# Kernel tuning notes

Measured on AMD Instinct MI355X. Metric: run time of the kernel, lower is better.

The kernel has to match this reference:

```python
import jax, jax.numpy as jnp
import numpy as np

B, S, D_IN, D_OUT, H = 4, 2048, 1024, 1024, 16
HD = D_OUT // H


def setup_inputs() -> dict:
    key = jax.random.key(0)
    ks = jax.random.split(key, 6)
    s = 1.0 / np.sqrt(D_IN)
    x = jax.random.normal(ks[0], (B, S, D_IN), dtype=jnp.float32)
    Wq = jax.random.uniform(ks[1], (D_OUT, D_IN), jnp.float32, -s, s)  # torch Linear weight [out,in]
    Wk = jax.random.uniform(ks[2], (D_OUT, D_IN), jnp.float32, -s, s)
    Wv = jax.random.uniform(ks[3], (D_OUT, D_IN), jnp.float32, -s, s)
    so = 1.0 / np.sqrt(D_OUT)
    Wo = jax.random.uniform(ks[4], (D_OUT, D_OUT), jnp.float32, -so, so)
    bo = jax.random.uniform(ks[5], (D_OUT,), jnp.float32, -so, so)
    return {"x": x, "Wq": Wq, "Wk": Wk, "Wv": Wv, "Wo": Wo, "bo": bo}


def reference(x, Wq, Wk, Wv, Wo, bo):
    b, n, _ = x.shape
    # projections (torch Linear: x @ W^T), split heads -> [b, h, n, hd]
    def heads(y):
        return y.reshape(b, n, H, HD).transpose(0, 2, 1, 3)
    q = heads(x @ Wq.T)
    k = heads(x @ Wk.T)
    v = heads(x @ Wv.T)
    scores = jnp.einsum('bhqd,bhkd->bhqk', q, k)
    causal = jnp.triu(jnp.ones((n, n), dtype=bool), k=1)
    scores = jnp.where(causal, -jnp.inf, scores)
    attn = jax.nn.softmax(scores / np.sqrt(HD), axis=-1)  # dropout p=0.0 -> identity
    ctx = jnp.einsum('bhqk,bhkd->bhqd', attn, v)
    ctx = ctx.transpose(0, 2, 1, 3).reshape(b, n, D_OUT)
    return ctx @ Wo.T + bo
```

## Files before the change

kernel.cpp:

```cpp
#include <hip/hip_runtime.h>
#include <hip/hip_bf16.h>
#include <stdint.h>

#define B_N 4
#define SEQ 2048
#define DMODEL 1024
#define NHEAD 16
#define HDIM 64
#define BHEADS (B_N * NHEAD)
#define MROWS (B_N * SEQ)

typedef short bf16x8_t __attribute__((ext_vector_type(8)));
typedef float f32x4_t __attribute__((ext_vector_type(4)));

static __device__ __forceinline__ unsigned short f2bf(float f) {
  __hip_bfloat16 h = __float2bfloat16(f);
  return __builtin_bit_cast(unsigned short, h);
}

#define GLDS16(gp, lp)                                                        \
  __builtin_amdgcn_global_load_lds(                                           \
      (const __attribute__((address_space(1))) unsigned int*)(gp),            \
      (__attribute__((address_space(3))) unsigned int*)(lp), 16, 0, 0)

__global__ void cast_f32_bf16_v4(const float* __restrict__ in,
                                 unsigned short* __restrict__ out, int n4,
                                 float scale) {
  int i = blockIdx.x * blockDim.x + threadIdx.x;
  if (i >= n4) return;
  float4 v = reinterpret_cast<const float4*>(in)[i];
  ushort4 o;
  o.x = f2bf(v.x * scale); o.y = f2bf(v.y * scale);
  o.z = f2bf(v.z * scale); o.w = f2bf(v.w * scale);
  reinterpret_cast<ushort4*>(out)[i] = o;
}

__global__ void cast_weights(const float* __restrict__ Wq,
                             const float* __restrict__ Wk,
                             const float* __restrict__ Wv,
                             const float* __restrict__ Wo,
                             unsigned short* __restrict__ out) {
  int i = blockIdx.x * blockDim.x + threadIdx.x;
  int mat = i >> 18;
  int off = i & 262143;
  const float* src = (mat == 0) ? Wq : (mat == 1) ? Wk : (mat == 2) ? Wv : Wo;
  float scale = (mat == 0) ? 0.125f : 1.0f;
  float4 v = reinterpret_cast<const float4*>(src)[off];
  ushort4 o;
  o.x = f2bf(v.x * scale); o.y = f2bf(v.y * scale);
  o.z = f2bf(v.z * scale); o.w = f2bf(v.w * scale);
  reinterpret_cast<ushort4*>(out)[i] = o;
}


#define SLOT_B 24576
#define NSLOT 5

#define GEMM_PIPE_LOOP(NHv)                                                   \
  int cur = 0, nxt = 3;                                                       \
  for (int h = 0; h < (NHv); ++h) {                                           \
    const char* cb = (const char*)smem + cur * SLOT_B;                        \
    bf16x8_t af[4], bfr[4];                                                   \
    _Pragma("unroll")                                                         \
    for (int rt = 0; rt < 4; rt++)                                            \
      af[rt] = *(const bf16x8_t*)(cb + offA[rt]);                             \
    _Pragma("unroll")                                                         \
    for (int ct = 0; ct < 4; ct++)                                            \
      bfr[ct] = *(const bf16x8_t*)(cb + offB[ct]);                            \
    if (h + 3 < (NHv)) {                                                      \
      char* sb = (char*)smem + nxt * SLOT_B;                                  \
      GLDS16(aB + (size_t)(h + 3) * 32, sb + t * 16);                         \
      GLDS16(b0B + (size_t)(h + 3) * 32, sb + 8192 + t * 16);                 \
      GLDS16(b1B + (size_t)(h + 3) * 32, sb + 16384 + t * 16);                \
    }                                                                         \
    __builtin_amdgcn_s_barrier();                                             \
    asm volatile("s_waitcnt lgkmcnt(0)" ::: "memory");                        \
    __builtin_amdgcn_s_setprio(1);                                            \
    _Pragma("unroll")                                                         \
    for (int rt = 0; rt < 4; rt++)                                            \
      _Pragma("unroll")                                                       \
      for (int ct = 0; ct < 4; ct++)                                          \
        acc[rt][ct] = __builtin_amdgcn_mfma_f32_16x16x32_bf16(                \
            af[rt], bfr[ct], acc[rt][ct], 0, 0, 0);                           \
    __builtin_amdgcn_s_setprio(0);                                            \
    if (h + 1 < (NHv)) {                                                      \
      if (h + 3 < (NHv))                                                      \
        asm volatile("s_waitcnt vmcnt(6)" ::: "memory");                      \
      else if (h + 2 < (NHv))                                                 \
        asm volatile("s_waitcnt vmcnt(3)" ::: "memory");                      \
      else                                                                    \
        asm volatile("s_waitcnt vmcnt(0)" ::: "memory");                      \
      __builtin_amdgcn_s_barrier();                                           \
    }                                                                         \
    if (++cur == NSLOT) cur = 0;                                              \
    if (++nxt == NSLOT) nxt = 0;                                              \
  }

__global__ __launch_bounds__(512, 2)
void gemm_qkv(const unsigned short* __restrict__ A,
              const unsigned short* __restrict__ W,
              unsigned short* __restrict__ Out) {
  __shared__ __align__(16) unsigned short smem[61440];

  const int t = threadIdx.x;
  const int lane = t & 63;
  const int w = t >> 6;
  const int quad = lane >> 4;
  const int l16 = lane & 15;
  const int rowBase = blockIdx.x * 128;
  const int colBase = blockIdx.y * 256;
  const int wr = (w >> 2) * 64;
  const int wc = (w & 3) * 64;
  const int K = DMODEL;
  const int NH = K / 32;

  const int srow = t >> 2;
  const int ssw = ((t & 3) ^ ((t >> 3) & 3)) * 8;
  const unsigned short* aB  = A + (size_t)(rowBase + srow) * K + ssw;
  const unsigned short* b0B = W + (size_t)(colBase + srow) * K + ssw;
  const unsigned short* b1B = W + (size_t)(colBase + 128 + srow) * K + ssw;

  const int swz = (quad ^ ((l16 >> 1) & 3)) * 16;
  int offA[4], offB[4];
#pragma unroll
  for (int rt = 0; rt < 4; rt++) offA[rt] = (wr + rt * 16 + l16) * 64 + swz;
#pragma unroll
  for (int ct = 0; ct < 4; ct++)
    offB[ct] = 8192 + (wc + ct * 16 + l16) * 64 + swz;

  f32x4_t zero4 = {0.f, 0.f, 0.f, 0.f};
  f32x4_t acc[4][4];
#pragma unroll
  for (int i = 0; i < 4; i++)
#pragma unroll
    for (int j = 0; j < 4; j++) acc[i][j] = zero4;

#pragma unroll
  for (int h = 0; h < 3; ++h) {
    char* sb = (char*)smem + h * SLOT_B;
    GLDS16(aB + h * 32, sb + t * 16);
    GLDS16(b0B + h * 32, sb + 8192 + t * 16);
    GLDS16(b1B + h * 32, sb + 16384 + t * 16);
  }
  asm volatile("s_waitcnt vmcnt(6)" ::: "memory");
  __builtin_amdgcn_s_barrier();

  GEMM_PIPE_LOOP(NH)

  __syncthreads();

  const int mat = colBase >> 10;
  const int nl = colBase & 1023;
  const int hh = (nl + wc) >> 6;
  const int bb = rowBase >> 11;

  if (mat == 2) {
    unsigned short* T = smem + w * 4608;
#pragma unroll
    for (int ct = 0; ct < 4; ct++)
#pragma unroll
      for (int rt = 0; rt < 4; rt++) {
        ushort4 pk;
        pk.x = f2bf(acc[rt][ct][0]);
        pk.y = f2bf(acc[rt][ct][1]);
        pk.z = f2bf(acc[rt][ct][2]);
        pk.w = f2bf(acc[rt][ct][3]);
        *(ushort4*)&T[(ct * 16 + l16) * 72 + rt * 16 + quad * 4] = pk;
      }
    const int srw = (rowBase & (SEQ - 1)) + wr;
    unsigned short* Cq = Out + 2 * (size_t)MROWS * DMODEL;
#pragma unroll
    for (int it = 0; it < 8; it++) {
      int nn = it * 8 + (lane >> 3);
      int sg = lane & 7;
      uint4 d = *(const uint4*)&T[nn * 72 + sg * 8];
      *(uint4*)(Cq + ((size_t)(bb * NHEAD + hh) * HDIM + nn) * SEQ + srw +
                sg * 8) = d;
    }
  } else {
    unsigned short* T = smem + w * 4608;
#pragma unroll
    for (int rt = 0; rt < 4; rt++)
#pragma unroll
      for (int ct = 0; ct < 4; ct++)
#pragma unroll
        for (int r = 0; r < 4; r++)
          T[(rt * 16 + quad * 4 + r) * 72 + ct * 16 + l16] =
              f2bf(acc[rt][ct][r]);
    unsigned short* Cq = Out + (size_t)mat * MROWS * DMODEL;
#pragma unroll
    for (int it = 0; it < 8; it++) {
      int idx = it * 64 + lane;
      int row = idx >> 3, sg = idx & 7, sgx = sg ^ (row & 7);
      uint4 d = *(const uint4*)&T[row * 72 + sgx * 8];
      int m = rowBase + wr + row;
      int s = m & (SEQ - 1), b = m >> 11;
      *(uint4*)(Cq + (((size_t)(b * NHEAD + hh)) * SEQ + s) * HDIM + sgx * 8) = d;
    }
  }
}

__global__ __launch_bounds__(512, 2)
void gemm_out(const unsigned short* __restrict__ A,
              const unsigned short* __restrict__ Bw,
              float* __restrict__ Cf, const float* __restrict__ bias) {
  __shared__ __align__(16) unsigned short smem[61440];

  const int t = threadIdx.x;
  const int lane = t & 63;
  const int w = t >> 6;
  const int quad = lane >> 4;
  const int l16 = lane & 15;
  const int rowBase = blockIdx.x * 128;
  const int colBase = blockIdx.y * 256;
  const int wr = (w >> 2) * 64;
  const int wc = (w & 3) * 64;
  const int K = DMODEL, N = DMODEL;
  const int NH = K / 32;

  const int srow = t >> 2;
  const int ssw = ((t & 3) ^ ((t >> 3) & 3)) * 8;
  const unsigned short* aB  = A + (size_t)(rowBase + srow) * K + ssw;
  const unsigned short* b0B = Bw + (size_t)(colBase + srow) * K + ssw;
  const unsigned short* b1B = Bw + (size_t)(colBase + 128 + srow) * K + ssw;

  const int swz = (quad ^ ((l16 >> 1) & 3)) * 16;
  int offA[4], offB[4];
#pragma unroll
  for (int rt = 0; rt < 4; rt++) offA[rt] = (wr + rt * 16 + l16) * 64 + swz;
#pragma unroll
  for (int ct = 0; ct < 4; ct++)
    offB[ct] = 8192 + (wc + ct * 16 + l16) * 64 + swz;

  f32x4_t zero4 = {0.f, 0.f, 0.f, 0.f};
  f32x4_t acc[4][4];
#pragma unroll
  for (int i = 0; i < 4; i++)
#pragma unroll
    for (int j = 0; j < 4; j++) acc[i][j] = zero4;

#pragma unroll
  for (int h = 0; h < 3; ++h) {
    char* sb = (char*)smem + h * SLOT_B;
    GLDS16(aB + h * 32, sb + t * 16);
    GLDS16(b0B + h * 32, sb + 8192 + t * 16);
    GLDS16(b1B + h * 32, sb + 16384 + t * 16);
  }
  asm volatile("s_waitcnt vmcnt(6)" ::: "memory");
  __builtin_amdgcn_s_barrier();

  GEMM_PIPE_LOOP(NH)

#pragma unroll
  for (int rt = 0; rt < 4; rt++)
#pragma unroll
    for (int ct = 0; ct < 4; ct++) {
      int n = colBase + wc + ct * 16 + l16;
      float bv = bias[n];
#pragma unroll
      for (int r = 0; r < 4; r++) {
        int m = rowBase + wr + rt * 16 + quad * 4 + r;
        Cf[(size_t)m * N + n] = acc[rt][ct][r] + bv;
      }
    }
}

__global__ __launch_bounds__(256, 3)
void attn_kernel(const unsigned short* __restrict__ Qg_,
                 const unsigned short* __restrict__ Kg_,
                 const unsigned short* __restrict__ Vtg_,
                 unsigned short* __restrict__ ctx) {
  __shared__ __align__(16) unsigned short Ks[2][4096];
  __shared__ __align__(16) unsigned short Vs[2][4096];
  __shared__ __align__(16) unsigned short Ps[4][2048];

  const int t = threadIdx.x;
  const int lane = t & 63, w = t >> 6;
  const int quad = lane >> 4, l16 = lane & 15;
  const int sw = l16 & 7;
  unsigned short* PsW = &Ps[w][0];

  const int rank = blockIdx.x;
  const int qt = 15 - (rank >> 6);
  const int bh = rank & 63;
  const int nt = 2 * qt + 2;
  const size_t base = (size_t)bh * SEQ * HDIM;

  const int r0 = t >> 3;
  const int s0 = ((t & 7) ^ (r0 & 7)) * 8;
  const int r1 = r0 + 32;

  const unsigned short* Kg = Kg_ + base;
  const unsigned short* Vg = Vtg_ + base;

  GLDS16(Kg + r0 * HDIM + s0, (char*)&Ks[0][0] + t * 16);
  GLDS16(Kg + r1 * HDIM + s0, (char*)&Ks[0][0] + t * 16 + 4096);
  GLDS16(Vg + (size_t)r0 * SEQ + s0, (char*)&Vs[0][0] + t * 16);
  GLDS16(Vg + (size_t)r1 * SEQ + s0, (char*)&Vs[0][0] + t * 16 + 4096);

  const int q0w = qt * 128 + w * 32;

  bf16x8_t qf[2][2];
#pragma unroll
  for (int q2 = 0; q2 < 2; q2++)
#pragma unroll
    for (int kh = 0; kh < 2; kh++)
      qf[q2][kh] = *(const bf16x8_t*)(Qg_ + base +
          (size_t)(q0w + q2 * 16 + l16) * HDIM + kh * 32 + quad * 8);

  float l_[2] = {0.f, 0.f};
  f32x4_t zero4 = {0.f, 0.f, 0.f, 0.f};
  f32x4_t o[2][4];
#pragma unroll
  for (int q2 = 0; q2 < 2; q2++)
#pragma unroll
    for (int dt = 0; dt < 4; dt++) o[q2][dt] = zero4;

  int buf = 0;
  for (int jt = 0; jt < nt; ++jt) {
    __syncthreads();
    if (jt + 1 < nt) {
      const unsigned short* Kg2 = Kg + (size_t)(jt + 1) * 64 * HDIM;
      const unsigned short* Vg2 = Vg + (jt + 1) * 64;
      char* kd = (char*)&Ks[buf ^ 1][0] + t * 16;
      char* vd = (char*)&Vs[buf ^ 1][0] + t * 16;
      GLDS16(Kg2 + r0 * HDIM + s0, kd);
      GLDS16(Kg2 + r1 * HDIM + s0, kd + 4096);
      GLDS16(Vg2 + (size_t)r0 * SEQ + s0, vd);
      GLDS16(Vg2 + (size_t)r1 * SEQ + s0, vd + 4096);
    }

    if (jt * 64 <= q0w + 31) {
      const unsigned short* Kb = &Ks[buf][0];
      const unsigned short* Vb = &Vs[buf][0];
      f32x4_t sc[2][4];
#pragma unroll
      for (int q2 = 0; q2 < 2; q2++)
#pragma unroll
        for (int kt = 0; kt < 4; kt++) sc[q2][kt] = zero4;

#pragma unroll
      for (int kt = 0; kt < 4; kt++)
#pragma unroll
        for (int kh = 0; kh < 2; kh++) {
          bf16x8_t kf = *(const bf16x8_t*)((const char*)Kb +
              ((kt * 16 + l16) * 64 + (((kh * 4 + quad) ^ sw) * 8)) * 2);
          sc[0][kt] = __builtin_amdgcn_mfma_f32_16x16x32_bf16(
              kf, qf[0][kh], sc[0][kt], 0, 0, 0);
          sc[1][kt] = __builtin_amdgcn_mfma_f32_16x16x32_bf16(
              kf, qf[1][kh], sc[1][kt], 0, 0, 0);
        }

      if (jt * 64 + 63 > q0w) {
#pragma unroll
        for (int q2 = 0; q2 < 2; q2++) {
          int q = q0w + q2 * 16 + l16;
#pragma unroll
          for (int kt = 0; kt < 4; kt++)
#pragma unroll
            for (int r = 0; r < 4; r++) {
              int key = jt * 64 + kt * 16 + quad * 4 + r;
              if (key > q) sc[q2][kt][r] = -3.0e38f;
            }
        }
      }

#pragma unroll
      for (int q2 = 0; q2 < 2; q2++) {
        float sum = 0.f;
#pragma unroll
        for (int kt = 0; kt < 4; kt++) {
          float p0 = __expf(sc[q2][kt][0]);
          float p1 = __expf(sc[q2][kt][1]);
          float p2 = __expf(sc[q2][kt][2]);
          float p3 = __expf(sc[q2][kt][3]);
          sum += p0 + p1 + p2 + p3;
          ushort4 pk;
          pk.x = f2bf(p0); pk.y = f2bf(p1); pk.z = f2bf(p2); pk.w = f2bf(p3);
          int u = (kt * 4 + quad) ^ ((l16 & 7) << 1);
          *(ushort4*)&PsW[q2 * 1024 + l16 * 64 + u * 4] = pk;
        }
        sum += __shfl_xor(sum, 16, 64);
        sum += __shfl_xor(sum, 32, 64);
        l_[q2] += sum;
      }

      bf16x8_t pf[2][2];
#pragma unroll
      for (int q2 = 0; q2 < 2; q2++)
#pragma unroll
        for (int kc = 0; kc < 2; kc++) {
          int u = (kc * 8 + quad * 2) ^ ((l16 & 7) << 1);
          pf[q2][kc] = *(const bf16x8_t*)&PsW[q2 * 1024 + l16 * 64 + u * 4];
        }
#pragma unroll
      for (int dt = 0; dt < 4; dt++)
#pragma unroll
        for (int kc = 0; kc < 2; kc++) {
          bf16x8_t vfrag = *(const bf16x8_t*)((const char*)Vb +
              ((dt * 16 + l16) * 64 + (((kc * 4 + quad) ^ sw) * 8)) * 2);
          o[0][dt] = __builtin_amdgcn_mfma_f32_16x16x32_bf16(
              vfrag, pf[0][kc], o[0][dt], 0, 0, 0);
          o[1][dt] = __builtin_amdgcn_mfma_f32_16x16x32_bf16(
              vfrag, pf[1][kc], o[1][dt], 0, 0, 0);
        }
    }
    buf ^= 1;
  }

  const int bidx = bh >> 4, h = bh & 15;
#pragma unroll
  for (int q2 = 0; q2 < 2; q2++) {
    float inv = 1.0f / l_[q2];
#pragma unroll
    for (int dt = 0; dt < 4; dt++) {
      ushort4 pk;
      pk.x = f2bf(o[q2][dt][0] * inv);
      pk.y = f2bf(o[q2][dt][1] * inv);
      pk.z = f2bf(o[q2][dt][2] * inv);
      pk.w = f2bf(o[q2][dt][3] * inv);
      int u = (dt * 4 + quad) ^ ((l16 & 7) << 1);
      *(ushort4*)&PsW[q2 * 1024 + l16 * 64 + u * 4] = pk;
    }
  }
  {
    int qq = lane >> 2, sg = lane & 3;
#pragma unroll
    for (int q2 = 0; q2 < 2; q2++) {
      int ua = (sg * 2) ^ ((qq & 7) << 1);
      int ub = (sg * 2 + 8) ^ ((qq & 7) << 1);
      uint4 da = *(const uint4*)&PsW[q2 * 1024 + qq * 64 + ua * 4];
      uint4 db = *(const uint4*)&PsW[q2 * 1024 + qq * 64 + ub * 4];
      size_t rowoff =
          ((size_t)(bidx * SEQ + q0w + q2 * 16 + qq)) * DMODEL + h * HDIM;
      *(uint4*)(ctx + rowoff + sg * 8) = da;
      *(uint4*)(ctx + rowoff + (sg + 4) * 8) = db;
    }
  }
}

extern "C" void kernel_launch(void* const* d_in, const int* in_sizes, int n_in,
                              void* d_out, int out_size, void* d_ws,
                              size_t ws_size, hipStream_t stream) {
  const float* x  = (const float*)d_in[0];
  const float* Wq = (const float*)d_in[1];
  const float* Wk = (const float*)d_in[2];
  const float* Wv = (const float*)d_in[3];
  const float* Wo = (const float*)d_in[4];
  const float* bo = (const float*)d_in[5];
  float* out = (float*)d_out;

  const size_t XE = (size_t)MROWS * DMODEL;
  const size_t WE = (size_t)DMODEL * DMODEL;

  unsigned short* xb   = (unsigned short*)d_ws;
  unsigned short* wqb  = xb + XE;
  unsigned short* wob  = wqb + 3 * WE;
  unsigned short* Qb   = wqb + 4 * WE;
  unsigned short* Kb   = Qb + XE;
  unsigned short* Vtb  = Kb + XE;
  unsigned short* ctxb = xb;

  cast_f32_bf16_v4<<<(int)(XE / 4 + 255) / 256, 256, 0, stream>>>(x, xb,
      (int)(XE / 4), 1.0f);
  cast_weights<<<(int)(4 * WE / 4 + 255) / 256, 256, 0, stream>>>(Wq, Wk, Wv,
      Wo, wqb);

  gemm_qkv<<<dim3(MROWS / 128, 3 * DMODEL / 256), 512, 0, stream>>>(xb, wqb, Qb);

  attn_kernel<<<dim3(1024), 256, 0, stream>>>(Qb, Kb, Vtb, ctxb);

  gemm_out<<<dim3(MROWS / 128, DMODEL / 256), 512, 0, stream>>>(ctxb, wob, out, bo);
}
```

Measured before the change: 229.9 us.

## Restructure GEMM main loop into ping-pong register-prefetch pipeline with 6 LDS slots

Replaces the per-iteration GEMM loop with a manually unrolled two-phase schedule: LDS fragments for the next K-step are read into a second register set while MFMAs run on the current set, and global->LDS loads are issued four steps ahead across six shared-memory slots. The aim is to hide LDS read latency and global load latency behind MFMA work, with one barrier per step instead of two. In exchange it uses more LDS (144 KB per block at 2 blocks/CU) and more VGPRs for the doubled fragments, which may pressure occupancy. The K-loop count is now hard-coded for K=1024.

```diff
diff --git a/kernel.cpp b/kernel.cpp
--- a/kernel.cpp
+++ b/kernel.cpp
@@ -54,53 +54,72 @@
 
 
 #define SLOT_B 24576
-#define NSLOT 5
-
-#define GEMM_PIPE_LOOP(NHv)                                                   \
-  int cur = 0, nxt = 3;                                                       \
-  for (int h = 0; h < (NHv); ++h) {                                           \
-    const char* cb = (const char*)smem + cur * SLOT_B;                        \
-    bf16x8_t af[4], bfr[4];                                                   \
+#define NSLOTS 6
+
+#define PH_READ(AFL, BFL)                                                     \
+  {                                                                           \
+    const char* cb = smem_c + rs * SLOT_B;                                    \
     _Pragma("unroll")                                                         \
     for (int rt = 0; rt < 4; rt++)                                            \
-      af[rt] = *(const bf16x8_t*)(cb + offA[rt]);                             \
+      AFL[rt] = *(const bf16x8_t*)(cb + offA[rt]);                            \
     _Pragma("unroll")                                                         \
     for (int ct = 0; ct < 4; ct++)                                            \
-      bfr[ct] = *(const bf16x8_t*)(cb + offB[ct]);                            \
-    if (h + 3 < (NHv)) {                                                      \
-      char* sb = (char*)smem + nxt * SLOT_B;                                  \
-      GLDS16(aB + (size_t)(h + 3) * 32, sb + t * 16);                         \
-      GLDS16(b0B + (size_t)(h + 3) * 32, sb + 8192 + t * 16);                 \
-      GLDS16(b1B + (size_t)(h + 3) * 32, sb + 16384 + t * 16);                \
-    }                                                                         \
-    __builtin_amdgcn_s_barrier();                                             \
-    asm volatile("s_waitcnt lgkmcnt(0)" ::: "memory");                        \
-    __builtin_amdgcn_s_setprio(1);                                            \
+      BFL[ct] = *(const bf16x8_t*)(cb + offB[ct]);                            \
+    if (++rs == NSLOTS) rs = 0;                                               \
+  }
+
+#define PH_GLDS(hh)                                                           \
+  {                                                                           \
+    char* sb = smem_c + gs * SLOT_B;                                          \
+    GLDS16(aB + (size_t)(hh) * 32, sb + t * 16);                              \
+    GLDS16(b0B + (size_t)(hh) * 32, sb + 8192 + t * 16);                      \
+    GLDS16(b1B + (size_t)(hh) * 32, sb + 16384 + t * 16);                     \
+    if (++gs == NSLOTS) gs = 0;                                               \
+  }
+
+#define PH_MFMA(AFU, BFU)                                                     \
+  __builtin_amdgcn_sched_barrier(0);                                          \
+  __builtin_amdgcn_s_setprio(1);                                              \
+  _Pragma("unroll")                                                           \
+  for (int rt = 0; rt < 4; rt++)                                              \
     _Pragma("unroll")                                                         \
-    for (int rt = 0; rt < 4; rt++)                                            \
-      _Pragma("unroll")                                                       \
-      for (int ct = 0; ct < 4; ct++)                                          \
-        acc[rt][ct] = __builtin_amdgcn_mfma_f32_16x16x32_bf16(                \
-            af[rt], bfr[ct], acc[rt][ct], 0, 0, 0);                           \
-    __builtin_amdgcn_s_setprio(0);                                            \
-    if (h + 1 < (NHv)) {                                                      \
-      if (h + 3 < (NHv))                                                      \
-        asm volatile("s_waitcnt vmcnt(6)" ::: "memory");                      \
-      else if (h + 2 < (NHv))                                                 \
-        asm volatile("s_waitcnt vmcnt(3)" ::: "memory");                      \
-      else                                                                    \
-        asm volatile("s_waitcnt vmcnt(0)" ::: "memory");                      \
-      __builtin_amdgcn_s_barrier();                                           \
-    }                                                                         \
-    if (++cur == NSLOT) cur = 0;                                              \
-    if (++nxt == NSLOT) nxt = 0;                                              \
-  }
+    for (int ct = 0; ct < 4; ct++)                                            \
+      acc[rt][ct] = __builtin_amdgcn_mfma_f32_16x16x32_bf16(                  \
+          AFU[rt], BFU[ct], acc[rt][ct], 0, 0, 0);                            \
+  __builtin_amdgcn_s_setprio(0);
+
+#define CERT(N)                                                               \
+  asm volatile("s_waitcnt vmcnt(" #N ")" ::: "memory");                       \
+  __builtin_amdgcn_s_barrier();                                               \
+  asm volatile("" ::: "memory");
+
+#define GEMM_PIPE_BODY                                                        \
+  _Pragma("unroll")                                                           \
+  for (int h = 0; h < 4; ++h) {                                               \
+    char* sb = smem_c + h * SLOT_B;                                           \
+    GLDS16(aB + (size_t)h * 32, sb + t * 16);                                 \
+    GLDS16(b0B + (size_t)h * 32, sb + 8192 + t * 16);                         \
+    GLDS16(b1B + (size_t)h * 32, sb + 16384 + t * 16);                        \
+  }                                                                           \
+  int rs = 0, gs = 4;                                                         \
+  bf16x8_t afX[4], bfX[4], afY[4], bfY[4];                                    \
+  CERT(9)                                                                     \
+  PH_READ(afX, bfX)                                                           \
+  for (int i = 0; i < 14; ++i) {                                              \
+    CERT(6) PH_READ(afY, bfY) PH_GLDS(2 * i + 4) PH_MFMA(afX, bfX)            \
+    CERT(6) PH_READ(afX, bfX) PH_GLDS(2 * i + 5) PH_MFMA(afY, bfY)            \
+  }                                                                           \
+  CERT(6) PH_READ(afY, bfY) PH_MFMA(afX, bfX)                   \
+  CERT(3) PH_READ(afX, bfX) PH_MFMA(afY, bfY)                   \
+  CERT(0) PH_READ(afY, bfY) PH_MFMA(afX, bfX)                   \
+  PH_MFMA(afY, bfY)
 
 __global__ __launch_bounds__(512, 2)
 void gemm_qkv(const unsigned short* __restrict__ A,
               const unsigned short* __restrict__ W,
               unsigned short* __restrict__ Out) {
-  __shared__ __align__(16) unsigned short smem[61440];
+  __shared__ __align__(16) unsigned short smem[73728];
+  char* smem_c = (char*)smem;
 
   const int t = threadIdx.x;
   const int lane = t & 63;
@@ -112,7 +131,6 @@
   const int wr = (w >> 2) * 64;
   const int wc = (w & 3) * 64;
   const int K = DMODEL;
-  const int NH = K / 32;
 
   const int srow = t >> 2;
   const int ssw = ((t & 3) ^ ((t >> 3) & 3)) * 8;
@@ -135,17 +153,7 @@
 #pragma unroll
     for (int j = 0; j < 4; j++) acc[i][j] = zero4;
 
-#pragma unroll
-  for (int h = 0; h < 3; ++h) {
-    char* sb = (char*)smem + h * SLOT_B;
-    GLDS16(aB + h * 32, sb + t * 16);
-    GLDS16(b0B + h * 32, sb + 8192 + t * 16);
-    GLDS16(b1B + h * 32, sb + 16384 + t * 16);
-  }
-  asm volatile("s_waitcnt vmcnt(6)" ::: "memory");
-  __builtin_amdgcn_s_barrier();
-
-  GEMM_PIPE_LOOP(NH)
+  GEMM_PIPE_BODY
 
   __syncthreads();
 
@@ -204,7 +212,8 @@
 void gemm_out(const unsigned short* __restrict__ A,
               const unsigned short* __restrict__ Bw,
               float* __restrict__ Cf, const float* __restrict__ bias) {
-  __shared__ __align__(16) unsigned short smem[61440];
+  __shared__ __align__(16) unsigned short smem[73728];
+  char* smem_c = (char*)smem;
 
   const int t = threadIdx.x;
   const int lane = t & 63;
@@ -216,7 +225,6 @@
   const int wr = (w >> 2) * 64;
   const int wc = (w & 3) * 64;
   const int K = DMODEL, N = DMODEL;
-  const int NH = K / 32;
 
   const int srow = t >> 2;
   const int ssw = ((t & 3) ^ ((t >> 3) & 3)) * 8;
@@ -239,17 +247,7 @@
 #pragma unroll
     for (int j = 0; j < 4; j++) acc[i][j] = zero4;
 
-#pragma unroll
-  for (int h = 0; h < 3; ++h) {
-    char* sb = (char*)smem + h * SLOT_B;
-    GLDS16(aB + h * 32, sb + t * 16);
-    GLDS16(b0B + h * 32, sb + 8192 + t * 16);
-    GLDS16(b1B + h * 32, sb + 16384 + t * 16);
-  }
-  asm volatile("s_waitcnt vmcnt(6)" ::: "memory");
-  __builtin_amdgcn_s_barrier();
-
-  GEMM_PIPE_LOOP(NH)
+  GEMM_PIPE_BODY
 
 #pragma unroll
   for (int rt = 0; rt < 4; rt++)
```

Measured after the change: 231.2 us. Within noise of the previous version (+0.6%).
